# Kernel optimization log

Measured on AMD Instinct MI355X. Metric: run time of the kernel, lower is better.

## Reference

```python
import jax, jax.numpy as jnp
import numpy as np

NBITS = 8
REDUCE = 64
OUT = 512


def setup_inputs() -> dict:
    key = jax.random.key(0)
    ks = jax.random.split(key, 6)
    T, B, C = 512, 16, 512
    ne = 2 ** NBITS
    x = jax.random.normal(ks[0], (T, B, C), dtype=jnp.float32)
    key_in = jax.random.normal(ks[1], (T, B, C), dtype=jnp.float32)  # unused by forward (overwritten)
    # xavier-ish init scales
    map_w = jax.random.normal(ks[2], (NBITS, C), dtype=jnp.float32) * np.sqrt(2.0 / (C + NBITS))
    map_b = jnp.zeros((NBITS,), dtype=jnp.float32)
    pw_w1 = jax.random.normal(ks[3], (REDUCE, C), dtype=jnp.float32) * np.sqrt(2.0 / (C + REDUCE))
    pw_w21 = jax.random.normal(ks[4], (ne, OUT * REDUCE), dtype=jnp.float32) * np.sqrt(2.0 / (ne + OUT * REDUCE))
    pw_w22 = jax.random.normal(ks[5], (ne, OUT * REDUCE), dtype=jnp.float32) * np.sqrt(2.0 / (ne + OUT * REDUCE))
    pw_B = jnp.zeros((1, 1, OUT), dtype=jnp.float32)
    return {"x": x, "key": key_in, "map_w": map_w, "map_b": map_b,
            "pw_w1": pw_w1, "pw_w21": pw_w21, "pw_w22": pw_w22, "pw_B": pw_B}


def reference(x, key, map_w, map_b, pw_w1, pw_w21, pw_w22, pw_B):
    # x: (T,B,C). `key` arg is overwritten by x in the original source.
    T, B, C = x.shape
    nbits = map_w.shape[0]
    out_dim = pw_B.shape[-1]
    reduce_dim = pw_w1.shape[0]

    k = x.reshape(T * B, C) @ map_w.T + map_b          # (T*B, nbits)
    z = jnp.clip(1.2 * jax.nn.sigmoid(k) - 0.1, 0.0, 1.0)  # saturated sigmoid
    code = (z > 0.5).astype(z.dtype)                   # eval: hard binary code

    pows = (2 ** jnp.arange(nbits, dtype=jnp.int32))   # bit_to_int weights
    qz1 = jnp.sum(code.astype(jnp.int32) * pows, axis=-1)          # (T*B,)
    qz2 = jnp.sum((1 - code.astype(jnp.int32)) * pows, axis=-1)    # (T*B,)

    # gather per-token expert rows and synthesize per-token weight matrix
    w2 = (pw_w21[qz1] + pw_w22[qz2]).reshape(T, B, out_dim, reduce_dim)

    # original computes (w2 @ pw_w1) @ x; reassociated as w2 @ (pw_w1 @ x)
    # to avoid materializing the (T,B,out,in) intermediate (same math)
    v = jnp.einsum('ri,tbi->tbr', pw_w1, x)            # (T,B,reduce)
    y = jnp.einsum('tbor,tbr->tbo', w2, v) + pw_B      # (T,B,out)

    loss = jnp.zeros((1,), dtype=x.dtype)
    return (y, loss)
```

## Files before the change

### kernel.cpp

```cpp
#include <hip/hip_runtime.h>

#define NTOK 8192
#define CDIM 512
#define NB   8
#define RD   64
#define OD   512

#define TPB_A 8
#define XPAD  4
#define XROW  (CDIM + XPAD)
#define XROW4 (XROW / 4)

typedef unsigned char u8;

__device__ __forceinline__ float4 f4add(float4 a, float4 b) {
    return make_float4(a.x + b.x, a.y + b.y, a.z + b.z, a.w + b.w);
}

__global__ __launch_bounds__(128) void phaseA(
    const float* __restrict__ x, const float* __restrict__ map_w,
    const float* __restrict__ map_b, const float* __restrict__ w1,
    u8* __restrict__ q_out, float* __restrict__ v_out,
    float* __restrict__ loss_out)
{
    const int t    = threadIdx.x;
    const int tok0 = blockIdx.x * TPB_A;
    __shared__ __align__(16) float xs[TPB_A * XROW];

    const float4* xsrc = (const float4*)(x + (size_t)tok0 * CDIM);
    #pragma unroll
    for (int i = t; i < TPB_A * (CDIM / 4); i += 128) {
        int r = i >> 7, c = i & 127;
        *((float4*)(xs + r * XROW) + c) = xsrc[i];
    }
    __syncthreads();

    {
        const int bit  = t & 7;
        const int half = (t >> 3) & 1;
        const int tk   = t >> 4;
        const float4* m4 = (const float4*)(map_w + (size_t)bit * CDIM) + half * 64;
        const float4* x4 = (const float4*)xs + tk * XROW4 + half * 64;
        double a0 = 0.0, a1 = 0.0;
        for (int j = 0; j < 64; ++j) {
            float4 m = m4[j], xv = x4[j];
            a0 += (double)m.x * (double)xv.x + (double)m.y * (double)xv.y;
            a1 += (double)m.z * (double)xv.z + (double)m.w * (double)xv.w;
        }
        double a = a0 + a1;
        a += __shfl_xor(a, 8);
        const double k = a + (double)map_b[bit];
        const unsigned long long m = __ballot(k > 0.0);
        if ((t & 15) == 0) {
            int g = (t >> 4) & 3;
            q_out[tok0 + tk] = (u8)((m >> (g * 16)) & 0xFFull);
        }
    }

    {
        const int r  = t & 63;
        const int tg = t >> 6;
        const float4* w4 = (const float4*)(w1 + (size_t)r * CDIM);
        const float4* xb = (const float4*)xs + (size_t)(tg * 4) * XROW4;
        float acc0 = 0.f, acc1 = 0.f, acc2 = 0.f, acc3 = 0.f;
        for (int j = 0; j < CDIM / 4; ++j) {
            float4 wv = w4[j];
            float4 x0 = xb[j];
            float4 x1 = xb[XROW4 + j];
            float4 x2 = xb[2 * XROW4 + j];
            float4 x3 = xb[3 * XROW4 + j];
            acc0 += wv.x * x0.x + wv.y * x0.y + wv.z * x0.z + wv.w * x0.w;
            acc1 += wv.x * x1.x + wv.y * x1.y + wv.z * x1.z + wv.w * x1.w;
            acc2 += wv.x * x2.x + wv.y * x2.y + wv.z * x2.z + wv.w * x2.w;
            acc3 += wv.x * x3.x + wv.y * x3.y + wv.z * x3.z + wv.w * x3.w;
        }
        float* vo = v_out + (size_t)(tok0 + tg * 4) * RD + r;
        vo[0 * RD] = acc0; vo[1 * RD] = acc1; vo[2 * RD] = acc2; vo[3 * RD] = acc3;
    }

    if (blockIdx.x == 0 && t == 0) loss_out[0] = 0.0f;
}

__global__ __launch_bounds__(128) void phaseB(
    const u8* __restrict__ q_arr, const float* __restrict__ v_arr,
    const float* __restrict__ w21, const float* __restrict__ w22,
    const float* __restrict__ pwB, float* __restrict__ y)
{
    const int q  = blockIdx.x >> 2;
    const int qu = blockIdx.x & 3;
    const int t  = threadIdx.x;
    const int o  = qu * 128 + t;

    __shared__ unsigned short list[NTOK];
    __shared__ int cnt;
    __shared__ __align__(16) float vs[8 * RD];

    const float4* pa = (const float4*)w21 + (size_t)q * (OD * RD / 4) + (size_t)o * (RD / 4);
    const float4* pb = (const float4*)w22 + (size_t)(255 - q) * (OD * RD / 4) + (size_t)o * (RD / 4);
    float4 a0 = pa[0],  a1 = pa[1],  a2 = pa[2],  a3 = pa[3],
           a4 = pa[4],  a5 = pa[5],  a6 = pa[6],  a7 = pa[7],
           a8 = pa[8],  a9 = pa[9],  a10 = pa[10], a11 = pa[11],
           a12 = pa[12], a13 = pa[13], a14 = pa[14], a15 = pa[15];
    float4 b0 = pb[0],  b1 = pb[1],  b2 = pb[2],  b3 = pb[3],
           b4 = pb[4],  b5 = pb[5],  b6 = pb[6],  b7 = pb[7],
           b8 = pb[8],  b9 = pb[9],  b10 = pb[10], b11 = pb[11],
           b12 = pb[12], b13 = pb[13], b14 = pb[14], b15 = pb[15];

    if (t == 0) cnt = 0;
    __syncthreads();

    const uint4* qa = (const uint4*)q_arr;
    for (int i = t; i < NTOK / 16; i += 128) {
        uint4 u = qa[i];
        int sbase = i * 16;
#define CHK(WORD, OFF) { unsigned uw = (WORD); \
        if ((int)(uw & 0xFFu)         == q) list[atomicAdd(&cnt, 1)] = (unsigned short)(sbase + (OFF));     \
        if ((int)((uw >> 8)  & 0xFFu) == q) list[atomicAdd(&cnt, 1)] = (unsigned short)(sbase + (OFF) + 1); \
        if ((int)((uw >> 16) & 0xFFu) == q) list[atomicAdd(&cnt, 1)] = (unsigned short)(sbase + (OFF) + 2); \
        if ((int)(uw >> 24)           == q) list[atomicAdd(&cnt, 1)] = (unsigned short)(sbase + (OFF) + 3); }
        CHK(u.x, 0) CHK(u.y, 4) CHK(u.z, 8) CHK(u.w, 12)
#undef CHK
    }
    __syncthreads();
    const int n = cnt;
    if (n == 0) return;

    float4 w0 = f4add(a0, b0),  w1 = f4add(a1, b1),  w2 = f4add(a2, b2),  w3 = f4add(a3, b3),
           w4 = f4add(a4, b4),  w5 = f4add(a5, b5),  w6 = f4add(a6, b6),  w7 = f4add(a7, b7),
           w8 = f4add(a8, b8),  w9 = f4add(a9, b9),  w10 = f4add(a10, b10), w11 = f4add(a11, b11),
           w12 = f4add(a12, b12), w13 = f4add(a13, b13), w14 = f4add(a14, b14), w15 = f4add(a15, b15);
    const float bias = pwB[o];

    const float4* v4 = (const float4*)v_arr;
    for (int base = 0; base < n; base += 8) {
        const int nb = min(8, n - base);
        if (t < nb * 16)
            ((float4*)vs)[t] = v4[(size_t)list[base + (t >> 4)] * (RD / 4) + (t & 15)];
        __syncthreads();
        int i = 0;
        for (; i + 2 <= nb; i += 2) {
            const float4* p0 = (const float4*)vs + (size_t)i * 16;
            const float4* p1 = p0 + 16;
            float acc0 = bias, acc1 = bias;
#define STEP(J, W) { float4 u0 = p0[J], u1 = p1[J]; \
            acc0 += W.x * u0.x + W.y * u0.y + W.z * u0.z + W.w * u0.w; \
            acc1 += W.x * u1.x + W.y * u1.y + W.z * u1.z + W.w * u1.w; }
            STEP(0, w0)  STEP(1, w1)  STEP(2, w2)  STEP(3, w3)
            STEP(4, w4)  STEP(5, w5)  STEP(6, w6)  STEP(7, w7)
            STEP(8, w8)  STEP(9, w9)  STEP(10, w10) STEP(11, w11)
            STEP(12, w12) STEP(13, w13) STEP(14, w14) STEP(15, w15)
#undef STEP
            y[(size_t)list[base + i]     * OD + o] = acc0;
            y[(size_t)list[base + i + 1] * OD + o] = acc1;
        }
        if (i < nb) {
            const float4* p0 = (const float4*)vs + (size_t)i * 16;
            float acc0 = bias;
#define STEP1(J, W) { float4 u0 = p0[J]; \
            acc0 += W.x * u0.x + W.y * u0.y + W.z * u0.z + W.w * u0.w; }
            STEP1(0, w0)  STEP1(1, w1)  STEP1(2, w2)  STEP1(3, w3)
            STEP1(4, w4)  STEP1(5, w5)  STEP1(6, w6)  STEP1(7, w7)
            STEP1(8, w8)  STEP1(9, w9)  STEP1(10, w10) STEP1(11, w11)
            STEP1(12, w12) STEP1(13, w13) STEP1(14, w14) STEP1(15, w15)
#undef STEP1
            y[(size_t)list[base + i] * OD + o] = acc0;
        }
        __syncthreads();
    }
}

__global__ __launch_bounds__(256) void mono(
    const float* __restrict__ x, const float* __restrict__ map_w,
    const float* __restrict__ map_b, const float* __restrict__ w1,
    const float* __restrict__ w21, const float* __restrict__ w22,
    const float* __restrict__ pwB, float* __restrict__ y)
{
    const int tok = blockIdx.x;
    const int t   = threadIdx.x;
    __shared__ float xsh[CDIM];
    __shared__ float vsh[RD];
    __shared__ int qsh;

    if (t == 0) qsh = 0;
    for (int i = t; i < CDIM; i += 256) xsh[i] = x[(size_t)tok * CDIM + i];
    __syncthreads();

    if (t < NB) {
        double a = 0.0;
        const float* mrow = map_w + (size_t)t * CDIM;
        for (int j = 0; j < CDIM; ++j) a += (double)mrow[j] * (double)xsh[j];
        a += (double)map_b[t];
        if (a > 0.0) atomicOr(&qsh, 1 << t);
    }
    if (t < RD) {
        const float* wrow = w1 + (size_t)t * CDIM;
        float acc = 0.f;
        for (int j = 0; j < CDIM; ++j) acc += wrow[j] * xsh[j];
        vsh[t] = acc;
    }
    __syncthreads();

    const int q = qsh;
    for (int o = t; o < OD; o += 256) {
        const float* pa = w21 + (size_t)q * (OD * RD) + (size_t)o * RD;
        const float* pb = w22 + (size_t)(255 - q) * (OD * RD) + (size_t)o * RD;
        float acc = pwB[o];
        for (int r = 0; r < RD; ++r) acc += (pa[r] + pb[r]) * vsh[r];
        y[(size_t)tok * OD + o] = acc;
    }
    if (tok == 0 && t == 0) y[(size_t)NTOK * OD] = 0.0f;
}

extern "C" void kernel_launch(void* const* d_in, const int* in_sizes, int n_in,
                              void* d_out, int out_size, void* d_ws, size_t ws_size,
                              hipStream_t stream) {
    const float* x     = (const float*)d_in[0];
    const float* map_w = (const float*)d_in[2];
    const float* map_b = (const float*)d_in[3];
    const float* w1    = (const float*)d_in[4];
    const float* w21   = (const float*)d_in[5];
    const float* w22   = (const float*)d_in[6];
    const float* pwB   = (const float*)d_in[7];
    float* out = (float*)d_out;

    const size_t need = (size_t)NTOK + (size_t)NTOK * RD * sizeof(float);
    if (ws_size >= need) {
        u8*    q_ws = (u8*)d_ws;
        float* v_ws = (float*)((char*)d_ws + NTOK);
        phaseA<<<NTOK / TPB_A, 128, 0, stream>>>(x, map_w, map_b, w1, q_ws, v_ws,
                                                 out + (size_t)NTOK * OD);
        phaseB<<<256 * 4, 128, 0, stream>>>(q_ws, v_ws, w21, w22, pwB, out);
    } else {
        mono<<<NTOK, 256, 0, stream>>>(x, map_w, map_b, w1, w21, w22, pwB, out);
    }
}
```

Before: 198.5 us.

## Shrink phaseA blocks, software-pipeline weight loads, and prefetch code bytes in phaseB

phaseA now runs one 64-thread wavefront per block over 4 tokens and preloads map_w and w1 rows into register arrays in double-buffered batches, so global loads overlap the FMAs. phaseB issues its loads of the token code array before the expert-weight loads and unrolls the scan over four fixed uint4 words per thread, and both kernels get min-blocks launch bounds. The aim is more memory-level parallelism and more blocks in phaseA, at the cost of heavier register pressure from the large register arrays, which could cause spills or lower occupancy.

```diff
diff --git a/kernel.cpp b/kernel.cpp
--- a/kernel.cpp
+++ b/kernel.cpp
@@ -6,7 +6,7 @@
 #define RD   64
 #define OD   512
 
-#define TPB_A 8
+#define TPB_A 4
 #define XPAD  4
 #define XROW  (CDIM + XPAD)
 #define XROW4 (XROW / 4)
@@ -16,8 +16,11 @@
 __device__ __forceinline__ float4 f4add(float4 a, float4 b) {
     return make_float4(a.x + b.x, a.y + b.y, a.z + b.z, a.w + b.w);
 }
-
-__global__ __launch_bounds__(128) void phaseA(
+__device__ __forceinline__ float dot4(float4 a, float4 b) {
+    return a.x * b.x + a.y * b.y + a.z * b.z + a.w * b.w;
+}
+
+__global__ __launch_bounds__(64, 2) void phaseA(
     const float* __restrict__ x, const float* __restrict__ map_w,
     const float* __restrict__ map_b, const float* __restrict__ w1,
     u8* __restrict__ q_out, float* __restrict__ v_out,
@@ -29,7 +32,7 @@
 
     const float4* xsrc = (const float4*)(x + (size_t)tok0 * CDIM);
     #pragma unroll
-    for (int i = t; i < TPB_A * (CDIM / 4); i += 128) {
+    for (int i = t; i < TPB_A * (CDIM / 4); i += 64) {
         int r = i >> 7, c = i & 127;
         *((float4*)(xs + r * XROW) + c) = xsrc[i];
     }
@@ -42,46 +45,67 @@
         const float4* m4 = (const float4*)(map_w + (size_t)bit * CDIM) + half * 64;
         const float4* x4 = (const float4*)xs + tk * XROW4 + half * 64;
         double a0 = 0.0, a1 = 0.0;
-        for (int j = 0; j < 64; ++j) {
-            float4 m = m4[j], xv = x4[j];
-            a0 += (double)m.x * (double)xv.x + (double)m.y * (double)xv.y;
-            a1 += (double)m.z * (double)xv.z + (double)m.w * (double)xv.w;
+        for (int b = 0; b < 8; ++b) {
+            float4 mb[8];
+            #pragma unroll
+            for (int i = 0; i < 8; ++i) mb[i] = m4[b * 8 + i];
+            #pragma unroll
+            for (int i = 0; i < 8; ++i) {
+                float4 m = mb[i], xv = x4[b * 8 + i];
+                a0 += (double)m.x * (double)xv.x + (double)m.y * (double)xv.y;
+                a1 += (double)m.z * (double)xv.z + (double)m.w * (double)xv.w;
+            }
         }
         double a = a0 + a1;
         a += __shfl_xor(a, 8);
         const double k = a + (double)map_b[bit];
         const unsigned long long m = __ballot(k > 0.0);
-        if ((t & 15) == 0) {
-            int g = (t >> 4) & 3;
-            q_out[tok0 + tk] = (u8)((m >> (g * 16)) & 0xFFull);
-        }
+        if ((t & 15) == 0)
+            q_out[tok0 + tk] = (u8)((m >> ((t >> 4) * 16)) & 0xFFull);
     }
 
     {
-        const int r  = t & 63;
-        const int tg = t >> 6;
+        const int r = t;
         const float4* w4 = (const float4*)(w1 + (size_t)r * CDIM);
-        const float4* xb = (const float4*)xs + (size_t)(tg * 4) * XROW4;
+        const float4* xq = (const float4*)xs;
         float acc0 = 0.f, acc1 = 0.f, acc2 = 0.f, acc3 = 0.f;
-        for (int j = 0; j < CDIM / 4; ++j) {
-            float4 wv = w4[j];
-            float4 x0 = xb[j];
-            float4 x1 = xb[XROW4 + j];
-            float4 x2 = xb[2 * XROW4 + j];
-            float4 x3 = xb[3 * XROW4 + j];
-            acc0 += wv.x * x0.x + wv.y * x0.y + wv.z * x0.z + wv.w * x0.w;
-            acc1 += wv.x * x1.x + wv.y * x1.y + wv.z * x1.z + wv.w * x1.w;
-            acc2 += wv.x * x2.x + wv.y * x2.y + wv.z * x2.z + wv.w * x2.w;
-            acc3 += wv.x * x3.x + wv.y * x3.y + wv.z * x3.z + wv.w * x3.w;
-        }
-        float* vo = v_out + (size_t)(tok0 + tg * 4) * RD + r;
+        float4 wa[16], wb[16];
+        #pragma unroll
+        for (int i = 0; i < 16; ++i) wa[i] = w4[i];
+        for (int b = 0; b < 8; b += 2) {
+            #pragma unroll
+            for (int i = 0; i < 16; ++i) wb[i] = w4[(b + 1) * 16 + i];
+            #pragma unroll
+            for (int i = 0; i < 16; ++i) {
+                const int j = b * 16 + i;
+                float4 wv = wa[i];
+                acc0 += dot4(wv, xq[j]);
+                acc1 += dot4(wv, xq[XROW4 + j]);
+                acc2 += dot4(wv, xq[2 * XROW4 + j]);
+                acc3 += dot4(wv, xq[3 * XROW4 + j]);
+            }
+            if (b < 6) {
+                #pragma unroll
+                for (int i = 0; i < 16; ++i) wa[i] = w4[(b + 2) * 16 + i];
+            }
+            #pragma unroll
+            for (int i = 0; i < 16; ++i) {
+                const int j = (b + 1) * 16 + i;
+                float4 wv = wb[i];
+                acc0 += dot4(wv, xq[j]);
+                acc1 += dot4(wv, xq[XROW4 + j]);
+                acc2 += dot4(wv, xq[2 * XROW4 + j]);
+                acc3 += dot4(wv, xq[3 * XROW4 + j]);
+            }
+        }
+        float* vo = v_out + (size_t)tok0 * RD + r;
         vo[0 * RD] = acc0; vo[1 * RD] = acc1; vo[2 * RD] = acc2; vo[3 * RD] = acc3;
     }
 
     if (blockIdx.x == 0 && t == 0) loss_out[0] = 0.0f;
 }
 
-__global__ __launch_bounds__(128) void phaseB(
+__global__ __launch_bounds__(128, 2) void phaseB(
     const u8* __restrict__ q_arr, const float* __restrict__ v_arr,
     const float* __restrict__ w21, const float* __restrict__ w22,
     const float* __restrict__ pwB, float* __restrict__ y)
@@ -94,6 +118,9 @@
     __shared__ unsigned short list[NTOK];
     __shared__ int cnt;
     __shared__ __align__(16) float vs[8 * RD];
+
+    const uint4* qa = (const uint4*)q_arr;
+    uint4 qv0 = qa[t], qv1 = qa[t + 128], qv2 = qa[t + 256], qv3 = qa[t + 384];
 
     const float4* pa = (const float4*)w21 + (size_t)q * (OD * RD / 4) + (size_t)o * (RD / 4);
     const float4* pb = (const float4*)w22 + (size_t)(255 - q) * (OD * RD / 4) + (size_t)o * (RD / 4);
@@ -109,18 +136,16 @@
     if (t == 0) cnt = 0;
     __syncthreads();
 
-    const uint4* qa = (const uint4*)q_arr;
-    for (int i = t; i < NTOK / 16; i += 128) {
-        uint4 u = qa[i];
-        int sbase = i * 16;
-#define CHK(WORD, OFF) { unsigned uw = (WORD); \
-        if ((int)(uw & 0xFFu)         == q) list[atomicAdd(&cnt, 1)] = (unsigned short)(sbase + (OFF));     \
-        if ((int)((uw >> 8)  & 0xFFu) == q) list[atomicAdd(&cnt, 1)] = (unsigned short)(sbase + (OFF) + 1); \
-        if ((int)((uw >> 16) & 0xFFu) == q) list[atomicAdd(&cnt, 1)] = (unsigned short)(sbase + (OFF) + 2); \
-        if ((int)(uw >> 24)           == q) list[atomicAdd(&cnt, 1)] = (unsigned short)(sbase + (OFF) + 3); }
-        CHK(u.x, 0) CHK(u.y, 4) CHK(u.z, 8) CHK(u.w, 12)
+#define CHK(WORD, SB, OFF) { unsigned uw = (WORD); \
+    if ((int)(uw & 0xFFu)         == q) list[atomicAdd(&cnt, 1)] = (unsigned short)((SB) + (OFF));     \
+    if ((int)((uw >> 8)  & 0xFFu) == q) list[atomicAdd(&cnt, 1)] = (unsigned short)((SB) + (OFF) + 1); \
+    if ((int)((uw >> 16) & 0xFFu) == q) list[atomicAdd(&cnt, 1)] = (unsigned short)((SB) + (OFF) + 2); \
+    if ((int)(uw >> 24)           == q) list[atomicAdd(&cnt, 1)] = (unsigned short)((SB) + (OFF) + 3); }
+    { int sb = t * 16;          CHK(qv0.x, sb, 0) CHK(qv0.y, sb, 4) CHK(qv0.z, sb, 8) CHK(qv0.w, sb, 12) }
+    { int sb = (t + 128) * 16;  CHK(qv1.x, sb, 0) CHK(qv1.y, sb, 4) CHK(qv1.z, sb, 8) CHK(qv1.w, sb, 12) }
+    { int sb = (t + 256) * 16;  CHK(qv2.x, sb, 0) CHK(qv2.y, sb, 4) CHK(qv2.z, sb, 8) CHK(qv2.w, sb, 12) }
+    { int sb = (t + 384) * 16;  CHK(qv3.x, sb, 0) CHK(qv3.y, sb, 4) CHK(qv3.z, sb, 8) CHK(qv3.w, sb, 12) }
 #undef CHK
-    }
     __syncthreads();
     const int n = cnt;
     if (n == 0) return;
@@ -227,8 +252,8 @@
     if (ws_size >= need) {
         u8*    q_ws = (u8*)d_ws;
         float* v_ws = (float*)((char*)d_ws + NTOK);
-        phaseA<<<NTOK / TPB_A, 128, 0, stream>>>(x, map_w, map_b, w1, q_ws, v_ws,
-                                                 out + (size_t)NTOK * OD);
+        phaseA<<<NTOK / TPB_A, 64, 0, stream>>>(x, map_w, map_b, w1, q_ws, v_ws,
+                                                out + (size_t)NTOK * OD);
         phaseB<<<256 * 4, 128, 0, stream>>>(q_ws, v_ws, w21, w22, pwB, out);
     } else {
         mono<<<NTOK, 256, 0, stream>>>(x, map_w, map_b, w1, w21, w22, pwB, out);
```

After: 323.6 us. +63.0%, slower.
